# Kernel tuning notes

Measured on AMD Instinct MI355X. Metric: run time of the kernel, lower is better.

## Reference

```python
import jax, jax.numpy as jnp
import numpy as np

EPS = 1e-5  # torch BatchNorm1d default eps


def _batchnorm(x, gamma, beta):
    # training-mode BatchNorm1d: biased batch statistics over the N dim
    mean = jnp.mean(x, axis=0)
    var = jnp.var(x, axis=0)
    return (x - mean) * jax.lax.rsqrt(var + EPS) * gamma + beta


def setup_inputs() -> dict:
    key = jax.random.key(0)
    ks = jax.random.split(key, 12)
    N_last, N_cur, E, F = 100000, 50000, 500000, 300
    Din = F + 3  # 303: neighbor features concat coord delta
    inp = {
        "last_coors": jax.random.normal(ks[0], (N_last, 3), jnp.float32),
        "last_features": jax.random.normal(ks[1], (N_last, F), jnp.float32),
        "current_coors": jax.random.normal(ks[2], (N_cur, 3), jnp.float32),
        "cur_idx": jax.random.randint(ks[3], (E,), 0, N_cur),
        "last_idx": jax.random.randint(ks[4], (E,), 0, N_last),
        # in_linear: Linear(303,300) + ReLU + BN(300)
        "W1": jax.random.normal(ks[5], (Din, F), jnp.float32) / np.sqrt(Din),
        "b1": jnp.zeros((F,), jnp.float32),
        "g1": jnp.ones((F,), jnp.float32),
        "be1": jnp.zeros((F,), jnp.float32),
        # out_linear: Linear(300,300) + ReLU + BN(300)
        "W2": jax.random.normal(ks[6], (F, F), jnp.float32) / np.sqrt(F),
        "b2": jnp.zeros((F,), jnp.float32),
        "g2": jnp.ones((F,), jnp.float32),
        "be2": jnp.zeros((F,), jnp.float32),
    }
    return inp


def reference(last_coors, last_features, current_coors, cur_idx, last_idx,
              W1, b1, g1, be1, W2, b2, g2, be2):
    N_cur = current_coors.shape[0]
    # gather: neighbor features + (neighbor - center) coordinate deltas -> [E, 303]
    edge_feats = jnp.concatenate(
        [last_features[last_idx], last_coors[last_idx] - current_coors[cur_idx]],
        axis=1)
    # in_linear MLP on edges
    h = _batchnorm(jnp.maximum(edge_feats @ W1 + b1, 0.0), g1, be1)  # [E, 300]
    # scatter-max aggregation to current-level nodes (empty segments -> 0,
    # matching torch_scatter.scatter(..., reduce='max') zero-init behavior)
    agg = jax.ops.segment_max(h, cur_idx, num_segments=N_cur)  # [N_cur, 300]
    agg = jnp.where(jnp.isfinite(agg), agg, 0.0)
    # out_linear MLP on nodes
    out = _batchnorm(jnp.maximum(agg @ W2 + b2, 0.0), g2, be2)
    return out
```

## Files before the change

### kernel.cpp

```cpp
#include <hip/hip_runtime.h>
#include <hip/hip_bf16.h>


#define NPART 64
#define SB 256
#define CH 256
#define STR 128
#define UNR 8

typedef __bf16 bf16_t;
typedef __bf16 bf16x4 __attribute__((ext_vector_type(4)));
typedef __bf16 bf16x8 __attribute__((ext_vector_type(8)));
typedef float f32x4 __attribute__((ext_vector_type(4)));

__device__ __forceinline__ unsigned enc_f32(float x) {
    unsigned u = __float_as_uint(x);
    return (u & 0x80000000u) ? ~u : (u | 0x80000000u);
}
__device__ __forceinline__ float dec_f32(unsigned e) {
    unsigned u = (e & 0x80000000u) ? (e & 0x7fffffffu) : ~e;
    return __uint_as_float(u);
}

__global__ void hist_k(const int* __restrict__ ci, int E, int* __restrict__ hist)
{
    const int e = blockIdx.x * 256 + threadIdx.x;
    if (e < E) atomicAdd(&hist[ci[e]], 1);
}

__global__ void scan_reduce(const int* __restrict__ hist, int nseg, int* __restrict__ bsum)
{
    __shared__ int s[SB];
    const int tid = threadIdx.x;
    const int i = blockIdx.x * SB + tid;
    s[tid] = (i < nseg) ? hist[i] : 0;
    __syncthreads();
    for (int o = SB / 2; o > 0; o >>= 1) {
        if (tid < o) s[tid] += s[tid + o];
        __syncthreads();
    }
    if (tid == 0) bsum[blockIdx.x] = s[0];
}

__global__ void scan_top(int* __restrict__ bsum, int nb)
{
    __shared__ int s[SB];
    const int tid = threadIdx.x;
    const int v = (tid < nb) ? bsum[tid] : 0;
    s[tid] = v;
    __syncthreads();
    for (int o = 1; o < SB; o <<= 1) {
        int x = 0;
        if (tid >= o) x = s[tid - o];
        __syncthreads();
        s[tid] += x;
        __syncthreads();
    }
    if (tid < nb) bsum[tid] = s[tid] - v;
}

__global__ void scan_final(const int* __restrict__ hist, int nseg,
                           const int* __restrict__ bsum, int* __restrict__ cnt)
{
    __shared__ int s[SB];
    const int tid = threadIdx.x;
    const int i = blockIdx.x * SB + tid;
    const int v = (i < nseg) ? hist[i] : 0;
    s[tid] = v;
    __syncthreads();
    for (int o = 1; o < SB; o <<= 1) {
        int x = 0;
        if (tid >= o) x = s[tid - o];
        __syncthreads();
        s[tid] += x;
        __syncthreads();
    }
    if (i < nseg) cnt[i] = s[tid] - v + bsum[blockIdx.x];
}

__global__ void scatter_k(const int* __restrict__ ci, const int* __restrict__ li,
                          int E, int* __restrict__ cnt, int2* __restrict__ sorted)
{
    const int e = blockIdx.x * 256 + threadIdx.x;
    if (e >= E) return;
    const int c = ci[e];
    const int pos = atomicAdd(&cnt[c], 1);
    sorted[pos] = make_int2(li[e], c);
}

__global__ void pack_wt(const float* __restrict__ W, bf16_t* __restrict__ WT)
{
    const int idx = blockIdx.x * 256 + threadIdx.x;
    if (idx >= 384 * 320) return;
    const int n = idx / 320, k = idx % 320;
    float v = (n < 300 && k < 300) ? W[k * 300 + n] : 0.f;
    WT[idx] = (bf16_t)v;
}

__global__ void cvt_lf(const float* __restrict__ lf, bf16_t* __restrict__ out, int M)
{
    const int idx = blockIdx.x * 256 + threadIdx.x;
    const int r = idx / 40, c8 = (idx % 40) * 8;
    if (r >= M) return;
    bf16x8 v = {};
    if (c8 + 8 <= 300) {
        const float4 a = *reinterpret_cast<const float4*>(&lf[(long)r * 300 + c8]);
        const float4 b = *reinterpret_cast<const float4*>(&lf[(long)r * 300 + c8 + 4]);
        v = (bf16x8){(bf16_t)a.x, (bf16_t)a.y, (bf16_t)a.z, (bf16_t)a.w,
                     (bf16_t)b.x, (bf16_t)b.y, (bf16_t)b.z, (bf16_t)b.w};
    } else if (c8 < 300) {
        const float4 a = *reinterpret_cast<const float4*>(&lf[(long)r * 300 + c8]);
        v[0] = (bf16_t)a.x; v[1] = (bf16_t)a.y; v[2] = (bf16_t)a.z; v[3] = (bf16_t)a.w;
    }
    *reinterpret_cast<bf16x8*>(&out[(long)r * 320 + c8]) = v;
}

template<int MODE>
__launch_bounds__(256)
__global__ void gemm_mfma(const bf16_t* __restrict__ A, int M,
                          const bf16_t* __restrict__ WT,
                          const float* __restrict__ bias,
                          bf16_t* __restrict__ outBF,
                          float* __restrict__ outF,
                          float* __restrict__ part)
{
    __shared__ bf16_t As[128][72];
    __shared__ bf16_t Bs[160][72];
    __shared__ float sSum[160], sSq[160];

    const int tid  = threadIdx.x;
    const int lane = tid & 63, wv = tid >> 6;
    const int wm = wv & 1, wn = wv >> 1;
    const int m0 = blockIdx.x * 128, n0 = blockIdx.y * 160;
    const int rl = lane & 15, quad = lane >> 4;

    if (MODE == 1 && tid < 160) { sSum[tid] = 0.f; sSq[tid] = 0.f; }

    f32x4 acc[4][5];
    #pragma unroll
    for (int i = 0; i < 4; ++i)
        #pragma unroll
        for (int j = 0; j < 5; ++j)
            acc[i][j] = (f32x4){0.f, 0.f, 0.f, 0.f};

    for (int k0 = 0; k0 < 320; k0 += 64) {
        #pragma unroll
        for (int i = 0; i < 4; ++i) {
            const int id = i * 256 + tid;
            const int r = id >> 3, kc = (id & 7) * 8;
            const int gr = min(m0 + r, M - 1);
            bf16x8 a8 = *reinterpret_cast<const bf16x8*>(&A[(long)gr * 320 + k0 + kc]);
            *reinterpret_cast<bf16x8*>(&As[r][kc]) = a8;
        }
        #pragma unroll
        for (int i = 0; i < 5; ++i) {
            const int id = i * 256 + tid;
            const int n = id >> 3, kc = (id & 7) * 8;
            bf16x8 w8 = *reinterpret_cast<const bf16x8*>(&WT[(long)(n0 + n) * 320 + k0 + kc]);
            *reinterpret_cast<bf16x8*>(&Bs[n][kc]) = w8;
        }
        __syncthreads();

        #pragma unroll
        for (int kk = 0; kk < 2; ++kk) {
            const int kb = kk * 32 + quad * 8;
            bf16x8 af[4], bfr[5];
            #pragma unroll
            for (int mi = 0; mi < 4; ++mi)
                af[mi] = *reinterpret_cast<const bf16x8*>(&As[wm * 64 + mi * 16 + rl][kb]);
            #pragma unroll
            for (int nj = 0; nj < 5; ++nj)
                bfr[nj] = *reinterpret_cast<const bf16x8*>(&Bs[wn * 80 + nj * 16 + rl][kb]);
            #pragma unroll
            for (int mi = 0; mi < 4; ++mi)
                #pragma unroll
                for (int nj = 0; nj < 5; ++nj)
                    acc[mi][nj] = __builtin_amdgcn_mfma_f32_16x16x32_bf16(
                        af[mi], bfr[nj], acc[mi][nj], 0, 0, 0);
        }
        __syncthreads();
    }

    if (MODE == 0) {
        #pragma unroll
        for (int mi = 0; mi < 4; ++mi)
            #pragma unroll
            for (int nj = 0; nj < 5; ++nj)
                #pragma unroll
                for (int reg = 0; reg < 4; ++reg) {
                    const int r = m0 + wm * 64 + mi * 16 + quad * 4 + reg;
                    const int c = n0 + wn * 80 + nj * 16 + rl;
                    if (r < M) {
                        const float v = (c < 300) ? (acc[mi][nj][reg] + bias[c]) : 0.f;
                        outBF[(long)r * 320 + c] = (bf16_t)v;
                    }
                }
    } else {
        float csum[5] = {}, csq[5] = {};
        #pragma unroll
        for (int mi = 0; mi < 4; ++mi)
            #pragma unroll
            for (int nj = 0; nj < 5; ++nj)
                #pragma unroll
                for (int reg = 0; reg < 4; ++reg) {
                    const int r = m0 + wm * 64 + mi * 16 + quad * 4 + reg;
                    const int c = n0 + wn * 80 + nj * 16 + rl;
                    if (r < M && c < 300) {
                        float v = fmaxf(acc[mi][nj][reg] + bias[c], 0.f);
                        outF[(long)r * 300 + c] = v;
                        csum[nj] += v; csq[nj] += v * v;
                    }
                }
        #pragma unroll
        for (int nj = 0; nj < 5; ++nj) {
            const int cl = wn * 80 + nj * 16 + rl;
            atomicAdd(&sSum[cl], csum[nj]);
            atomicAdd(&sSq[cl], csq[nj]);
        }
        __syncthreads();
        const int slot = (blockIdx.x + blockIdx.y * gridDim.x) & (NPART - 1);
        if (tid < 160 && (n0 + tid) < 300) {
            atomicAdd(&part[slot * 600 + n0 + tid], sSum[tid]);
            atomicAdd(&part[slot * 600 + 300 + n0 + tid], sSq[tid]);
        }
    }
}

__launch_bounds__(320)
__global__ void edge_pass(const bf16_t* __restrict__ Gb,
                          const float* __restrict__ last_coors,
                          const float* __restrict__ cur_coors,
                          const int2* __restrict__ sorted,
                          const float* __restrict__ Wc,
                          const float* __restrict__ g1,
                          unsigned* __restrict__ zbuf,
                          float* __restrict__ part1,
                          int E)
{
    __shared__ int sRow[CH], sCi[CH];
    __shared__ float sD0[CH], sD1[CH], sD2[CH];

    const int tid = threadIdx.x;
    const int e0 = blockIdx.x * CH;
    const int ecnt = min(CH, E - e0);

    for (int i = tid; i < ecnt; i += 320) {
        const int2 r = sorted[e0 + i];
        sRow[i] = r.x * 320;
        sCi[i]  = r.y;
        sD0[i] = last_coors[r.x * 3 + 0] - cur_coors[r.y * 3 + 0];
        sD1[i] = last_coors[r.x * 3 + 1] - cur_coors[r.y * 3 + 1];
        sD2[i] = last_coors[r.x * 3 + 2] - cur_coors[r.y * 3 + 2];
    }
    __syncthreads();

    const int stream = tid / 160;
    const int ft = (tid % 160) * 2;
    const bool real = (ft < 300);
    float w00 = 0.f, w01 = 0.f, w10 = 0.f, w11 = 0.f, w20 = 0.f, w21 = 0.f;
    float sgn0 = 1.f, sgn1 = 1.f;
    if (real) {
        w00 = Wc[ft];        w01 = Wc[ft + 1];
        w10 = Wc[300 + ft];  w11 = Wc[300 + ft + 1];
        w20 = Wc[600 + ft];  w21 = Wc[600 + ft + 1];
        sgn0 = (g1[ft]     < 0.f) ? -1.f : 1.f;
        sgn1 = (g1[ft + 1] < 0.f) ? -1.f : 1.f;
    }

    const int ibeg = stream * STR;
    const int iend = min(ecnt, ibeg + STR);

    int cur = (ibeg < iend) ? sCi[ibeg] : 0;
    float m0 = -3.4e38f, m1 = -3.4e38f;
    float sum0 = 0.f, sq0 = 0.f, sum1 = 0.f, sq1 = 0.f;

    int i = ibeg;
    for (; i + UNR <= iend; i += UNR) {
        unsigned gu[UNR];
        #pragma unroll
        for (int j = 0; j < UNR; ++j)
            gu[j] = *reinterpret_cast<const unsigned*>(&Gb[(long)sRow[i + j] + ft]);
        #pragma unroll
        for (int j = 0; j < UNR; ++j) {
            const int ci = sCi[i + j];
            if (ci != cur) {
                if (real) {
                    atomicMax(&zbuf[(long)cur * 320 + ft],     enc_f32(m0));
                    atomicMax(&zbuf[(long)cur * 320 + ft + 1], enc_f32(m1));
                }
                cur = ci;
                m0 = -3.4e38f; m1 = -3.4e38f;
            }
            const float g0 = __uint_as_float(gu[j] << 16);
            const float g1v = __uint_as_float(gu[j] & 0xffff0000u);
            const float d0 = sD0[i + j], d1 = sD1[i + j], d2 = sD2[i + j];
            const float y0 = fmaxf(g0  + d0 * w00 + d1 * w10 + d2 * w20, 0.f);
            const float y1 = fmaxf(g1v + d0 * w01 + d1 * w11 + d2 * w21, 0.f);
            sum0 += y0; sq0 += y0 * y0; m0 = fmaxf(m0, sgn0 * y0);
            sum1 += y1; sq1 += y1 * y1; m1 = fmaxf(m1, sgn1 * y1);
        }
    }
    for (; i < iend; ++i) {
        const int ci = sCi[i];
        if (ci != cur) {
            if (real) {
                atomicMax(&zbuf[(long)cur * 320 + ft],     enc_f32(m0));
                atomicMax(&zbuf[(long)cur * 320 + ft + 1], enc_f32(m1));
            }
            cur = ci;
            m0 = -3.4e38f; m1 = -3.4e38f;
        }
        const unsigned gu = *reinterpret_cast<const unsigned*>(&Gb[(long)sRow[i] + ft]);
        const float g0 = __uint_as_float(gu << 16);
        const float g1v = __uint_as_float(gu & 0xffff0000u);
        const float d0 = sD0[i], d1 = sD1[i], d2 = sD2[i];
        const float y0 = fmaxf(g0  + d0 * w00 + d1 * w10 + d2 * w20, 0.f);
        const float y1 = fmaxf(g1v + d0 * w01 + d1 * w11 + d2 * w21, 0.f);
        sum0 += y0; sq0 += y0 * y0; m0 = fmaxf(m0, sgn0 * y0);
        sum1 += y1; sq1 += y1 * y1; m1 = fmaxf(m1, sgn1 * y1);
    }
    if (real && ibeg < iend) {
        atomicMax(&zbuf[(long)cur * 320 + ft],     enc_f32(m0));
        atomicMax(&zbuf[(long)cur * 320 + ft + 1], enc_f32(m1));
    }

    const int slot = blockIdx.x & (NPART - 1);
    if (real) {
        atomicAdd(&part1[slot * 600 + ft],           sum0);
        atomicAdd(&part1[slot * 600 + ft + 1],       sum1);
        atomicAdd(&part1[slot * 600 + 300 + ft],     sq0);
        atomicAdd(&part1[slot * 600 + 300 + ft + 1], sq1);
    }
}

__global__ void stats_finalize(const float* __restrict__ part,
                               const float* __restrict__ g,
                               const float* __restrict__ be,
                               float invCnt, float* __restrict__ ac)
{
    const int t = threadIdx.x;
    if (t >= 300) return;
    float sum = 0.f, sq = 0.f;
    for (int p = 0; p < NPART; ++p) {
        sum += part[p * 600 + t];
        sq  += part[p * 600 + 300 + t];
    }
    const float mean = sum * invCnt;
    const float var = fmaxf(sq * invCnt - mean * mean, 0.f);
    const float inv = rsqrtf(var + 1e-5f);
    const float a = g[t] * inv;
    ac[t] = a;
    ac[300 + t] = be[t] - mean * a;
}

__global__ void agg_finalize(const unsigned* __restrict__ zbuf,
                             const float* __restrict__ ac1,
                             bf16_t* __restrict__ Ab2)
{
    const int t = threadIdx.x;
    float v = 0.f;
    if (t < 300) {
        const unsigned u = zbuf[(long)blockIdx.x * 320 + t];
        if (u != 0u) v = fabsf(ac1[t]) * dec_f32(u) + ac1[300 + t];
    }
    Ab2[(long)blockIdx.x * 320 + t] = (bf16_t)v;
}

__global__ void finalize_out(float* __restrict__ out,
                             const float* __restrict__ ac2)
{
    const int t = threadIdx.x;
    if (t >= 300) return;
    const long i = (long)blockIdx.x * 300 + t;
    out[i] = ac2[t] * out[i] + ac2[300 + t];
}

extern "C" void kernel_launch(void* const* d_in, const int* in_sizes, int n_in,
                              void* d_out, int out_size, void* d_ws, size_t ws_size,
                              hipStream_t stream)
{
    const float* last_coors    = (const float*)d_in[0];
    const float* last_features = (const float*)d_in[1];
    const float* cur_coors     = (const float*)d_in[2];
    const int*   cur_idx       = (const int*)d_in[3];
    const int*   last_idx      = (const int*)d_in[4];
    const float* W1  = (const float*)d_in[5];
    const float* b1  = (const float*)d_in[6];
    const float* g1  = (const float*)d_in[7];
    const float* be1 = (const float*)d_in[8];
    const float* W2  = (const float*)d_in[9];
    const float* b2  = (const float*)d_in[10];
    const float* g2  = (const float*)d_in[11];
    const float* be2 = (const float*)d_in[12];
    float* out = (float*)d_out;

    const int N_last = in_sizes[0] / 3;
    const int N_cur  = in_sizes[2] / 3;
    const int E      = in_sizes[3];

    const int nb1 = (N_cur + SB - 1) / SB;

    char* ws = (char*)d_ws;
    size_t off = 0;
    const size_t sz_r0 = (size_t)N_last * 320 * 2;
    bf16_t* Gb  = (bf16_t*)(ws + off);
    bf16_t* Ab2 = (bf16_t*)(ws + off);
    off += sz_r0; off = (off + 255) & ~(size_t)255;
    const size_t sz_alf = (size_t)N_last * 320 * 2;
    const size_t sz_zb  = (size_t)N_cur * 320 * 4;
    bf16_t* Alf = (bf16_t*)(ws + off);
    unsigned* zbuf = (unsigned*)(ws + off);
    off += (sz_alf > sz_zb ? sz_alf : sz_zb); off = (off + 255) & ~(size_t)255;
    int2* sorted = (int2*)(ws + off);  off += (size_t)E * 8;
    int* hist = (int*)(ws + off);      off += (size_t)nb1 * SB * 4;
    int* cnt  = (int*)(ws + off);      off += (size_t)nb1 * SB * 4;
    int* bsum = (int*)(ws + off);      off += 256 * 4;
    bf16_t* WT1 = (bf16_t*)(ws + off); off += (size_t)384 * 320 * 2;
    bf16_t* WT2 = (bf16_t*)(ws + off); off += (size_t)384 * 320 * 2;
    float* part1 = (float*)(ws + off); off += (size_t)NPART * 600 * 4;
    float* part2 = (float*)(ws + off); off += (size_t)NPART * 600 * 4;
    float* ac1   = (float*)(ws + off); off += 600 * 4;
    float* ac2   = (float*)(ws + off); off += 600 * 4;

    hipMemsetAsync(hist, 0, (size_t)nb1 * SB * 4, stream);
    hipMemsetAsync(part1, 0, (size_t)NPART * 600 * 4, stream);
    hipMemsetAsync(part2, 0, (size_t)NPART * 600 * 4, stream);

    hist_k<<<(E + 255) / 256, 256, 0, stream>>>(cur_idx, E, hist);
    scan_reduce<<<nb1, SB, 0, stream>>>(hist, N_cur, bsum);
    scan_top<<<1, SB, 0, stream>>>(bsum, nb1);
    scan_final<<<nb1, SB, 0, stream>>>(hist, N_cur, bsum, cnt);
    scatter_k<<<(E + 255) / 256, 256, 0, stream>>>(cur_idx, last_idx, E, cnt, sorted);

    pack_wt<<<480, 256, 0, stream>>>(W1, WT1);
    pack_wt<<<480, 256, 0, stream>>>(W2, WT2);
    cvt_lf<<<((N_last * 40) + 255) / 256, 256, 0, stream>>>(last_features, Alf, N_last);

    dim3 gridG((N_last + 127) / 128, 2);
    gemm_mfma<0><<<gridG, 256, 0, stream>>>(Alf, N_last, WT1, b1, Gb, nullptr, nullptr);

    hipMemsetAsync(zbuf, 0, sz_zb, stream);

    const int nEB = (E + CH - 1) / CH;
    edge_pass<<<nEB, 320, 0, stream>>>(Gb, last_coors, cur_coors, sorted,
                                       W1 + 300 * 300, g1, zbuf, part1, E);

    stats_finalize<<<1, 320, 0, stream>>>(part1, g1, be1, 1.0f / (float)E, ac1);
    agg_finalize<<<N_cur, 320, 0, stream>>>(zbuf, ac1, Ab2);

    dim3 grid2((N_cur + 127) / 128, 2);
    gemm_mfma<1><<<grid2, 256, 0, stream>>>(Ab2, N_cur, WT2, b2, nullptr, out, part2);

    stats_finalize<<<1, 320, 0, stream>>>(part2, g2, be2, 1.0f / (float)N_cur, ac2);
    finalize_out<<<N_cur, 320, 0, stream>>>(out, ac2);
}
```

Measured before the change: 622.7 us.

## Partition edge pass by destination segments and replace atomicMax with plain stores

```diff
diff --git a/kernel.cpp b/kernel.cpp
--- a/kernel.cpp
+++ b/kernel.cpp
@@ -4,8 +4,8 @@
 
 #define NPART 64
 #define SB 256
-#define CH 256
-#define STR 128
+#define SEGB 32
+#define CHS 256
 #define UNR 8
 
 typedef __bf16 bf16_t;
@@ -231,31 +231,36 @@
                           const float* __restrict__ last_coors,
                           const float* __restrict__ cur_coors,
                           const int2* __restrict__ sorted,
+                          const int*  __restrict__ segEnd,
                           const float* __restrict__ Wc,
                           const float* __restrict__ g1,
                           unsigned* __restrict__ zbuf,
                           float* __restrict__ part1,
-                          int E)
-{
-    __shared__ int sRow[CH], sCi[CH];
-    __shared__ float sD0[CH], sD1[CH], sD2[CH];
+                          int N_cur)
+{
+    __shared__ int sRow[2][CHS], sCi[2][CHS];
+    __shared__ float sD0[2][CHS], sD1[2][CHS], sD2[2][CHS];
 
     const int tid = threadIdx.x;
-    const int e0 = blockIdx.x * CH;
-    const int ecnt = min(CH, E - e0);
-
-    for (int i = tid; i < ecnt; i += 320) {
-        const int2 r = sorted[e0 + i];
-        sRow[i] = r.x * 320;
-        sCi[i]  = r.y;
-        sD0[i] = last_coors[r.x * 3 + 0] - cur_coors[r.y * 3 + 0];
-        sD1[i] = last_coors[r.x * 3 + 1] - cur_coors[r.y * 3 + 1];
-        sD2[i] = last_coors[r.x * 3 + 2] - cur_coors[r.y * 3 + 2];
-    }
-    __syncthreads();
-
-    const int stream = tid / 160;
-    const int ft = (tid % 160) * 2;
+    const int st  = (tid >= 160) ? 1 : 0;
+    const int ts  = tid - st * 160;
+
+    const int g0   = blockIdx.x * SEGB;
+    const int gEnd = min(g0 + SEGB, N_cur);
+    const int gMid = min(g0 + SEGB / 2, gEnd);
+
+    const int e00 = (g0   == 0) ? 0 : segEnd[g0 - 1];
+    const int e01 = (gMid == 0) ? 0 : segEnd[gMid - 1];
+    const int e11 = (gEnd == 0) ? 0 : segEnd[gEnd - 1];
+
+    const int ebeg = st ? e01 : e00;
+    const int eend = st ? e11 : e01;
+
+    const int nch0 = (e01 - e00 + CHS - 1) / CHS;
+    const int nch1 = (e11 - e01 + CHS - 1) / CHS;
+    const int nch  = max(nch0, nch1);
+
+    const int ft = ts * 2;
     const bool real = (ft < 300);
     float w00 = 0.f, w01 = 0.f, w10 = 0.f, w11 = 0.f, w20 = 0.f, w21 = 0.f;
     float sgn0 = 1.f, sgn1 = 1.f;
@@ -267,61 +272,74 @@
         sgn1 = (g1[ft + 1] < 0.f) ? -1.f : 1.f;
     }
 
-    const int ibeg = stream * STR;
-    const int iend = min(ecnt, ibeg + STR);
-
-    int cur = (ibeg < iend) ? sCi[ibeg] : 0;
+    int cur = -1;
     float m0 = -3.4e38f, m1 = -3.4e38f;
     float sum0 = 0.f, sq0 = 0.f, sum1 = 0.f, sq1 = 0.f;
 
-    int i = ibeg;
-    for (; i + UNR <= iend; i += UNR) {
-        unsigned gu[UNR];
-        #pragma unroll
-        for (int j = 0; j < UNR; ++j)
-            gu[j] = *reinterpret_cast<const unsigned*>(&Gb[(long)sRow[i + j] + ft]);
-        #pragma unroll
-        for (int j = 0; j < UNR; ++j) {
-            const int ci = sCi[i + j];
+    for (int ch = 0; ch < nch; ++ch) {
+        const int cbeg = ebeg + ch * CHS;
+        const int ccnt = min(CHS, eend - cbeg);
+
+        for (int i = ts; i < ccnt; i += 160) {
+            const int2 r = sorted[cbeg + i];
+            sRow[st][i] = r.x * 320;
+            sCi[st][i]  = r.y;
+            sD0[st][i] = last_coors[r.x * 3 + 0] - cur_coors[r.y * 3 + 0];
+            sD1[st][i] = last_coors[r.x * 3 + 1] - cur_coors[r.y * 3 + 1];
+            sD2[st][i] = last_coors[r.x * 3 + 2] - cur_coors[r.y * 3 + 2];
+        }
+        __syncthreads();
+
+        int i = 0;
+        for (; i + UNR <= ccnt; i += UNR) {
+            unsigned gu[UNR];
+            #pragma unroll
+            for (int j = 0; j < UNR; ++j)
+                gu[j] = *reinterpret_cast<const unsigned*>(&Gb[(long)sRow[st][i + j] + ft]);
+            #pragma unroll
+            for (int j = 0; j < UNR; ++j) {
+                const int ci = sCi[st][i + j];
+                if (ci != cur) {
+                    if (cur >= 0) {
+                        zbuf[(long)cur * 320 + ft]     = enc_f32(m0);
+                        zbuf[(long)cur * 320 + ft + 1] = enc_f32(m1);
+                    }
+                    cur = ci;
+                    m0 = -3.4e38f; m1 = -3.4e38f;
+                }
+                const float gx = __uint_as_float(gu[j] << 16);
+                const float gy = __uint_as_float(gu[j] & 0xffff0000u);
+                const float d0 = sD0[st][i + j], d1 = sD1[st][i + j], d2 = sD2[st][i + j];
+                const float y0 = fmaxf(gx + d0 * w00 + d1 * w10 + d2 * w20, 0.f);
+                const float y1 = fmaxf(gy + d0 * w01 + d1 * w11 + d2 * w21, 0.f);
+                sum0 += y0; sq0 += y0 * y0; m0 = fmaxf(m0, sgn0 * y0);
+                sum1 += y1; sq1 += y1 * y1; m1 = fmaxf(m1, sgn1 * y1);
+            }
+        }
+        for (; i < ccnt; ++i) {
+            const int ci = sCi[st][i];
             if (ci != cur) {
-                if (real) {
-                    atomicMax(&zbuf[(long)cur * 320 + ft],     enc_f32(m0));
-                    atomicMax(&zbuf[(long)cur * 320 + ft + 1], enc_f32(m1));
+                if (cur >= 0) {
+                    zbuf[(long)cur * 320 + ft]     = enc_f32(m0);
+                    zbuf[(long)cur * 320 + ft + 1] = enc_f32(m1);
                 }
                 cur = ci;
                 m0 = -3.4e38f; m1 = -3.4e38f;
             }
-            const float g0 = __uint_as_float(gu[j] << 16);
-            const float g1v = __uint_as_float(gu[j] & 0xffff0000u);
-            const float d0 = sD0[i + j], d1 = sD1[i + j], d2 = sD2[i + j];
-            const float y0 = fmaxf(g0  + d0 * w00 + d1 * w10 + d2 * w20, 0.f);
-            const float y1 = fmaxf(g1v + d0 * w01 + d1 * w11 + d2 * w21, 0.f);
+            const unsigned gu = *reinterpret_cast<const unsigned*>(&Gb[(long)sRow[st][i] + ft]);
+            const float gx = __uint_as_float(gu << 16);
+            const float gy = __uint_as_float(gu & 0xffff0000u);
+            const float d0 = sD0[st][i], d1 = sD1[st][i], d2 = sD2[st][i];
+            const float y0 = fmaxf(gx + d0 * w00 + d1 * w10 + d2 * w20, 0.f);
+            const float y1 = fmaxf(gy + d0 * w01 + d1 * w11 + d2 * w21, 0.f);
             sum0 += y0; sq0 += y0 * y0; m0 = fmaxf(m0, sgn0 * y0);
             sum1 += y1; sq1 += y1 * y1; m1 = fmaxf(m1, sgn1 * y1);
         }
-    }
-    for (; i < iend; ++i) {
-        const int ci = sCi[i];
-        if (ci != cur) {
-            if (real) {
-                atomicMax(&zbuf[(long)cur * 320 + ft],     enc_f32(m0));
-                atomicMax(&zbuf[(long)cur * 320 + ft + 1], enc_f32(m1));
-            }
-            cur = ci;
-            m0 = -3.4e38f; m1 = -3.4e38f;
-        }
-        const unsigned gu = *reinterpret_cast<const unsigned*>(&Gb[(long)sRow[i] + ft]);
-        const float g0 = __uint_as_float(gu << 16);
-        const float g1v = __uint_as_float(gu & 0xffff0000u);
-        const float d0 = sD0[i], d1 = sD1[i], d2 = sD2[i];
-        const float y0 = fmaxf(g0  + d0 * w00 + d1 * w10 + d2 * w20, 0.f);
-        const float y1 = fmaxf(g1v + d0 * w01 + d1 * w11 + d2 * w21, 0.f);
-        sum0 += y0; sq0 += y0 * y0; m0 = fmaxf(m0, sgn0 * y0);
-        sum1 += y1; sq1 += y1 * y1; m1 = fmaxf(m1, sgn1 * y1);
-    }
-    if (real && ibeg < iend) {
-        atomicMax(&zbuf[(long)cur * 320 + ft],     enc_f32(m0));
-        atomicMax(&zbuf[(long)cur * 320 + ft + 1], enc_f32(m1));
+        __syncthreads();
+    }
+    if (cur >= 0) {
+        zbuf[(long)cur * 320 + ft]     = enc_f32(m0);
+        zbuf[(long)cur * 320 + ft + 1] = enc_f32(m1);
     }
 
     const int slot = blockIdx.x & (NPART - 1);
@@ -441,9 +459,9 @@
 
     hipMemsetAsync(zbuf, 0, sz_zb, stream);
 
-    const int nEB = (E + CH - 1) / CH;
-    edge_pass<<<nEB, 320, 0, stream>>>(Gb, last_coors, cur_coors, sorted,
-                                       W1 + 300 * 300, g1, zbuf, part1, E);
+    const int nSB = (N_cur + SEGB - 1) / SEGB;
+    edge_pass<<<nSB, 320, 0, stream>>>(Gb, last_coors, cur_coors, sorted, cnt,
+                                       W1 + 300 * 300, g1, zbuf, part1, N_cur);
 
     stats_finalize<<<1, 320, 0, stream>>>(part1, g1, be1, 1.0f / (float)E, ac1);
     agg_finalize<<<N_cur, 320, 0, stream>>>(zbuf, ac1, Ab2);
```

New measurement: 586.3 us. 1.06x faster.
